# Performance work log

Hardware: AMD Instinct MI355X
Metric: run time of the kernel (lower is better)

The kernel has to match this reference:

```python
import jax, jax.numpy as jnp
import numpy as np

DIM = 384
DIM_HEAD = 32
HEADS = DIM // DIM_HEAD  # 12
WIN = 8
DIM_FF = 1536
FUSED = DIM + DIM + DIM_FF  # 2304


def setup_inputs() -> dict:
    key = jax.random.key(0)
    ks = jax.random.split(key, 8)
    B, H, W = 16, 64, 64
    x = jax.random.normal(ks[0], (B, DIM, H, W), dtype=jnp.float32)
    s = lambda fan_in: 1.0 / np.sqrt(fan_in)
    w_fused = jax.random.normal(ks[1], (FUSED, DIM), dtype=jnp.float32) * s(DIM)
    w_gate = jax.random.normal(ks[2], (HEADS, DIM), dtype=jnp.float32) * s(DIM)
    b_gate = jnp.full((HEADS,), 0.5, dtype=jnp.float32)  # init_constant_(0.5)
    w_attn_out = jax.random.normal(ks[3], (DIM, DIM), dtype=jnp.float32) * s(DIM)
    w_ff_out = jax.random.normal(ks[4], (DIM, DIM_FF), dtype=jnp.float32) * s(DIM_FF)
    # StarReLU learnable scalars (metaformer defaults)
    sr_scale = jnp.asarray(0.8944, dtype=jnp.float32)
    sr_bias = jnp.asarray(-0.4472, dtype=jnp.float32)
    return {"x": x, "w_fused": w_fused, "w_gate": w_gate, "b_gate": b_gate,
            "w_attn_out": w_attn_out, "w_ff_out": w_ff_out,
            "sr_scale": sr_scale, "sr_bias": sr_bias}


def reference(x, w_fused, w_gate, b_gate, w_attn_out, w_ff_out, sr_scale, sr_bias):
    B, C, H, W = x.shape
    p = WIN
    gh, gw = H // p, W // p
    n = p * p
    # b c (h p1) (w p2) -> (b h w) (p1 p2) c
    xw = x.reshape(B, C, gh, p, gw, p).transpose(0, 2, 4, 3, 5, 1).reshape(B * gh * gw, n, C)
    fused = jnp.einsum('bnc,fc->bnf', xw, w_fused)  # [Bw, n, 2304]
    q, kv, x_ff = jnp.split(fused, [DIM, 2 * DIM], axis=-1)
    # b n (h d) -> b h n d
    q = q.reshape(-1, n, HEADS, DIM_HEAD).transpose(0, 2, 1, 3)
    kv = kv.reshape(-1, n, HEADS, DIM_HEAD).transpose(0, 2, 1, 3)
    scale = 1.0 / np.sqrt(DIM_HEAD)
    scores = jnp.einsum('bhnd,bhmd->bhnm', q, kv) * scale
    attn = jax.nn.softmax(scores, axis=-1)
    x_attn = jnp.einsum('bhnm,bhmd->bhnd', attn, kv)  # kv is both key and value
    gate = jnp.einsum('bnc,hc->bnh', xw, w_gate) + b_gate  # [Bw, n, heads]
    x_attn = x_attn * jax.nn.sigmoid(gate.transpose(0, 2, 1)[..., None])
    x_attn = x_attn.transpose(0, 2, 1, 3).reshape(-1, n, DIM)
    ff = sr_scale * jnp.square(jax.nn.relu(x_ff)) + sr_bias  # StarReLU
    out = jnp.einsum('bnc,oc->bno', x_attn, w_attn_out) + jnp.einsum('bnf,of->bno', ff, w_ff_out)
    # (b h w) (p1 p2) c -> b c (h p1) (w p2)
    out = out.reshape(B, gh, gw, p, p, C).transpose(0, 5, 1, 3, 2, 4).reshape(B, C, H, W)
    return out
```

## Files before the change

kernel.cpp:

```cpp
#include <hip/hip_runtime.h>
#include <hip/hip_bf16.h>

typedef __bf16 bf16x8 __attribute__((ext_vector_type(8), may_alias));
typedef float f32x4 __attribute__((ext_vector_type(4), may_alias));
typedef unsigned short ushort_a __attribute__((may_alias));

#define MFMA(a, b, c) __builtin_amdgcn_mfma_f32_16x16x32_bf16(a, b, c, 0, 0, 0)

__device__ __forceinline__ unsigned short f2bf(float f) {
  return __builtin_bit_cast(unsigned short, (__bf16)f);
}


__global__ __launch_bounds__(256) void prep_weights(
    const float* __restrict__ wf, const float* __restrict__ wg,
    const float* __restrict__ wao, const float* __restrict__ wfo,
    unsigned short* __restrict__ ws) {
  int i = blockIdx.x * 256 + threadIdx.x;
  if (i < 884736) { ws[i] = f2bf(wf[i]); return; }
  int j = i - 884736;
  if (j < 6144) { ws[i] = f2bf(j < 4608 ? wg[j] : 0.0f); return; }
  j -= 6144;
  if (j < 147456) { ws[i] = f2bf(wao[j]); return; }
  j -= 147456;
  if (j < 589824) ws[i] = f2bf(wfo[j]);
}


__global__ __launch_bounds__(512, 2) void fused_main(
    const float* __restrict__ x,
    const float* __restrict__ bgate,
    const float* __restrict__ srs,
    const float* __restrict__ srb,
    const unsigned short* __restrict__ wsb,
    float* __restrict__ out) {
  const unsigned short* wfB  = wsb;
  const unsigned short* wgB  = wsb + 884736;
  const unsigned short* waoB = wsb + 890880;
  const unsigned short* wfoB = wsb + 1038336;

  __shared__ __align__(16) char smem[114688];
  char* As  = smem;
  char* Stg = smem + 98304;

  const int tid = threadIdx.x;
  const int lane = tid & 63, wave = tid >> 6;
  const int l15 = lane & 15, l4 = lane >> 4;
  const int pair = wave >> 1, nb = (wave & 1) * 32;
  char* PB  = smem + 49152 + pair * 12288;
  char* KTb = PB + 8192;

  const int g  = blockIdx.x;
  const int wi = (g & 7) * 128 + (g >> 3);
  const int b = wi >> 6, ghi = (wi >> 3) & 7, gwi = wi & 7;
  const int h0 = ghi * 8, w0 = gwi * 8;

  {
    const float* xb = x + (size_t)b * 1572864 + h0 * 64 + w0;
    for (int it = 0; it < 6; ++it) {
      int idx = it * 512 + tid;
      int c = idx % 384, p1 = idx / 384;
      const float* src = xb + (size_t)c * 4096 + p1 * 64;
      float4 v0 = *(const float4*)src;
      float4 v1 = *(const float4*)(src + 4);
      float f[8] = {v0.x, v0.y, v0.z, v0.w, v1.x, v1.y, v1.z, v1.w};
#pragma unroll
      for (int jj = 0; jj < 8; ++jj) {
        int row = p1 * 8 + jj;
        int byte = (row * 768 + c * 2) ^ ((row & 7) << 4);
        *(ushort_a*)(As + byte) = f2bf(f[jj]);
      }
    }
  }
  const float ss = srs[0], sbi = srb[0];
  __syncthreads();

  auto ldA = [&](int row, int ks) -> bf16x8 {
    int byte = (row * 768 + ks * 64 + l4 * 16) ^ ((row & 7) << 4);
    return *(const bf16x8*)(As + byte);
  };

  f32x4 gfr[2] = {};
  {
    const unsigned short* wg0 = wgB + (size_t)l15 * 384 + l4 * 8;
#pragma unroll 2
    for (int ks = 0; ks < 12; ++ks) {
      bf16x8 bg = *(const bf16x8*)(wg0 + ks * 32);
      bf16x8 a0 = ldA(nb + l15, ks), a1 = ldA(nb + 16 + l15, ks);
      gfr[0] = MFMA(a0, bg, gfr[0]);
      gfr[1] = MFMA(a1, bg, gfr[1]);
    }
    float gb = (l15 < 12) ? bgate[l15] : 0.0f;
    gfr[0] += gb;
    gfr[1] += gb;
  }

  f32x4 of[4][3] = {};

#pragma unroll 1
  for (int r = 0; r < 3; ++r) {
    const int h = r * 4 + pair;
    f32x4 qf[2][2] = {}, kf[2][2] = {};
    const unsigned short* wq = wfB + ((size_t)(h * 32) + l15) * 384 + l4 * 8;
    const unsigned short* wk = wq + (size_t)384 * 384;
#pragma unroll 2
    for (int ks = 0; ks < 12; ++ks) {
      bf16x8 a0 = ldA(nb + l15, ks), a1 = ldA(nb + 16 + l15, ks);
#pragma unroll
      for (int nt = 0; nt < 2; ++nt) {
        bf16x8 bq = *(const bf16x8*)(wq + (size_t)nt * 16 * 384 + ks * 32);
        bf16x8 bk = *(const bf16x8*)(wk + (size_t)nt * 16 * 384 + ks * 32);
        qf[0][nt] = MFMA(a0, bq, qf[0][nt]);
        qf[1][nt] = MFMA(a1, bq, qf[1][nt]);
        kf[0][nt] = MFMA(a0, bk, kf[0][nt]);
        kf[1][nt] = MFMA(a1, bk, kf[1][nt]);
      }
    }
#pragma unroll
    for (int mt = 0; mt < 2; ++mt)
#pragma unroll
      for (int nt = 0; nt < 2; ++nt)
#pragma unroll
        for (int rr = 0; rr < 4; ++rr) {
          int n = nb + mt * 16 + l4 * 4 + rr;
          int d = nt * 16 + l15;
          int sw = (n & 7) << 4;
          *(ushort_a*)(PB + ((n * 128 + d * 2) ^ sw)) =
              f2bf(qf[mt][nt][rr] * 0.176776695f);
          unsigned short kvv = f2bf(kf[mt][nt][rr]);
          *(ushort_a*)(PB + ((n * 128 + 64 + d * 2) ^ sw)) = kvv;
          *(ushort_a*)(KTb + ((d * 128 + n * 2) ^ ((d & 7) << 4))) = kvv;
        }
    __syncthreads();
    f32x4 sf[2][4] = {};
    {
      bf16x8 bkv[4];
#pragma unroll
      for (int ni = 0; ni < 4; ++ni) {
        int m = ni * 16 + l15;
        bkv[ni] = *(const bf16x8*)(PB + ((m * 128 + 64 + l4 * 16) ^ ((m & 7) << 4)));
      }
#pragma unroll
      for (int mt = 0; mt < 2; ++mt) {
        int n = nb + mt * 16 + l15;
        bf16x8 aq = *(const bf16x8*)(PB + ((n * 128 + l4 * 16) ^ ((n & 7) << 4)));
#pragma unroll
        for (int ni = 0; ni < 4; ++ni) sf[mt][ni] = MFMA(aq, bkv[ni], sf[mt][ni]);
      }
    }
    __syncthreads();
#pragma unroll
    for (int mt = 0; mt < 2; ++mt) {
#pragma unroll
      for (int rr = 0; rr < 4; ++rr) {
        float v0 = sf[mt][0][rr], v1 = sf[mt][1][rr],
              v2 = sf[mt][2][rr], v3 = sf[mt][3][rr];
        float mx = fmaxf(fmaxf(v0, v1), fmaxf(v2, v3));
        mx = fmaxf(mx, __shfl_xor(mx, 1, 64));
        mx = fmaxf(mx, __shfl_xor(mx, 2, 64));
        mx = fmaxf(mx, __shfl_xor(mx, 4, 64));
        mx = fmaxf(mx, __shfl_xor(mx, 8, 64));
        float e0 = __expf(v0 - mx), e1 = __expf(v1 - mx),
              e2 = __expf(v2 - mx), e3 = __expf(v3 - mx);
        float sm = e0 + e1 + e2 + e3;
        sm += __shfl_xor(sm, 1, 64);
        sm += __shfl_xor(sm, 2, 64);
        sm += __shfl_xor(sm, 4, 64);
        sm += __shfl_xor(sm, 8, 64);
        float rs = 1.0f / sm;
        int n = nb + mt * 16 + l4 * 4 + rr;
        int base = n * 128, sw = (n & 7) << 4;
        *(ushort_a*)(PB + ((base + l15 * 2) ^ sw))      = f2bf(e0 * rs);
        *(ushort_a*)(PB + ((base + 32 + l15 * 2) ^ sw)) = f2bf(e1 * rs);
        *(ushort_a*)(PB + ((base + 64 + l15 * 2) ^ sw)) = f2bf(e2 * rs);
        *(ushort_a*)(PB + ((base + 96 + l15 * 2) ^ sw)) = f2bf(e3 * rs);
      }
    }
    f32x4 xo[2][2] = {};
#pragma unroll
    for (int ks = 0; ks < 2; ++ks) {
      bf16x8 bv[2];
#pragma unroll
      for (int nt = 0; nt < 2; ++nt) {
        int d = nt * 16 + l15;
        bv[nt] = *(const bf16x8*)(KTb + ((d * 128 + ks * 64 + l4 * 16) ^ ((d & 7) << 4)));
      }
#pragma unroll
      for (int mt = 0; mt < 2; ++mt) {
        int n = nb + mt * 16 + l15;
        bf16x8 ap = *(const bf16x8*)(PB + ((n * 128 + ks * 64 + l4 * 16) ^ ((n & 7) << 4)));
        xo[mt][0] = MFMA(ap, bv[0], xo[mt][0]);
        xo[mt][1] = MFMA(ap, bv[1], xo[mt][1]);
      }
    }
#pragma unroll
    for (int mt = 0; mt < 2; ++mt) {
#pragma unroll
      for (int rr = 0; rr < 4; ++rr) {
        float gv = __shfl(gfr[mt][rr], (lane & 48) | h, 64);
        float sg = 1.0f / (1.0f + __expf(-gv));
        int n = nb + mt * 16 + l4 * 4 + rr;
        int sw = (n & 7) << 4;
        int c0 = pair * 32 + l15;
        *(ushort_a*)(Stg + ((n * 256 + c0 * 2) ^ sw))        = f2bf(xo[mt][0][rr] * sg);
        *(ushort_a*)(Stg + ((n * 256 + (c0 + 16) * 2) ^ sw)) = f2bf(xo[mt][1][rr] * sg);
      }
    }
    __syncthreads();
    {
      const unsigned short* wao0 =
          waoB + (size_t)(wave * 48 + l15) * 384 + r * 128 + l4 * 8;
#pragma unroll
      for (int ks = 0; ks < 4; ++ks) {
        int kb = ks * 64 + l4 * 16, sz = (l15 & 7) << 4;
        bf16x8 a0 = *(const bf16x8*)(Stg + ((l15 * 256 + kb) ^ sz));
        bf16x8 a1 = *(const bf16x8*)(Stg + (((16 + l15) * 256 + kb) ^ sz));
        bf16x8 a2 = *(const bf16x8*)(Stg + (((32 + l15) * 256 + kb) ^ sz));
        bf16x8 a3 = *(const bf16x8*)(Stg + (((48 + l15) * 256 + kb) ^ sz));
#pragma unroll
        for (int nt = 0; nt < 3; ++nt) {
          bf16x8 bw = *(const bf16x8*)(wao0 + (size_t)nt * 16 * 384 + ks * 32);
          of[0][nt] = MFMA(a0, bw, of[0][nt]);
          of[1][nt] = MFMA(a1, bw, of[1][nt]);
          of[2][nt] = MFMA(a2, bw, of[2][nt]);
          of[3][nt] = MFMA(a3, bw, of[3][nt]);
        }
      }
    }
  }

#pragma unroll 1
  for (int t = 0; t < 12; ++t) {
    f32x4 ffr[4] = {};
    const unsigned short* wfin =
        wfB + (size_t)(768 + t * 128 + wave * 16 + l15) * 384 + l4 * 8;
#pragma unroll 2
    for (int ks = 0; ks < 12; ++ks) {
      bf16x8 a0 = ldA(l15, ks), a1 = ldA(16 + l15, ks),
             a2 = ldA(32 + l15, ks), a3 = ldA(48 + l15, ks);
      bf16x8 bw = *(const bf16x8*)(wfin + ks * 32);
      ffr[0] = MFMA(a0, bw, ffr[0]);
      ffr[1] = MFMA(a1, bw, ffr[1]);
      ffr[2] = MFMA(a2, bw, ffr[2]);
      ffr[3] = MFMA(a3, bw, ffr[3]);
    }
    char* fb = smem + 49152 + (t & 1) * 16384;
#pragma unroll
    for (int mt = 0; mt < 4; ++mt)
#pragma unroll
      for (int rr = 0; rr < 4; ++rr) {
        float v = fmaxf(ffr[mt][rr], 0.0f);
        v = ss * v * v + sbi;
        int n = mt * 16 + l4 * 4 + rr;
        int cw = wave * 16 + l15;
        *(ushort_a*)(fb + ((n * 256 + cw * 2) ^ ((n & 7) << 4))) = f2bf(v);
      }
    __syncthreads();
    const unsigned short* wfo2 =
        wfoB + (size_t)(wave * 48 + l15) * 1536 + t * 128 + l4 * 8;
#pragma unroll
    for (int ks = 0; ks < 4; ++ks) {
      int kb = ks * 64 + l4 * 16, sz = (l15 & 7) << 4;
      bf16x8 a0 = *(const bf16x8*)(fb + ((l15 * 256 + kb) ^ sz));
      bf16x8 a1 = *(const bf16x8*)(fb + (((16 + l15) * 256 + kb) ^ sz));
      bf16x8 a2 = *(const bf16x8*)(fb + (((32 + l15) * 256 + kb) ^ sz));
      bf16x8 a3 = *(const bf16x8*)(fb + (((48 + l15) * 256 + kb) ^ sz));
#pragma unroll
      for (int nt = 0; nt < 3; ++nt) {
        bf16x8 bw = *(const bf16x8*)(wfo2 + (size_t)nt * 16 * 1536 + ks * 32);
        of[0][nt] = MFMA(a0, bw, of[0][nt]);
        of[1][nt] = MFMA(a1, bw, of[1][nt]);
        of[2][nt] = MFMA(a2, bw, of[2][nt]);
        of[3][nt] = MFMA(a3, bw, of[3][nt]);
      }
    }
  }

  float* ob = out + (size_t)b * 1572864 + h0 * 64 + w0;
#pragma unroll
  for (int nt = 0; nt < 3; ++nt) {
    int col = wave * 48 + nt * 16 + l15;
    float* oc = ob + (size_t)col * 4096;
#pragma unroll
    for (int mt = 0; mt < 4; ++mt) {
      int n0 = mt * 16 + l4 * 4;
      *(f32x4*)(oc + (n0 >> 3) * 64 + (n0 & 7)) = of[mt][nt];
    }
  }
}

extern "C" void kernel_launch(void* const* d_in, const int* in_sizes, int n_in,
                              void* d_out, int out_size, void* d_ws, size_t ws_size,
                              hipStream_t stream) {
  const float* x   = (const float*)d_in[0];
  const float* wf  = (const float*)d_in[1];
  const float* wg  = (const float*)d_in[2];
  const float* bg  = (const float*)d_in[3];
  const float* wao = (const float*)d_in[4];
  const float* wfo = (const float*)d_in[5];
  const float* srs = (const float*)d_in[6];
  const float* srb = (const float*)d_in[7];
  unsigned short* ws = (unsigned short*)d_ws;

  prep_weights<<<6360, 256, 0, stream>>>(wf, wg, wao, wfo, ws);
  fused_main<<<1024, 512, 0, stream>>>(x, bg, srs, srb, ws, (float*)d_out);
}
```

Measured before the change: 563.8 us.

## Repartition waves to two heads per round and shrink LDS for higher occupancy

Attention now assigns four waves per head, each handling 16 rows, and processes two heads per round over six rounds instead of four heads over three. The staging buffer shrinks to 64 columns per round, cutting shared memory from 112KB to 80KB, and launch bounds are raised to allow more blocks per CU. The output projection tiles change to 32 rows by 96 columns per wave, which cuts LDS A-fragment reads but doubles the weight fragments loaded per wave. This costs more rounds and barriers for the attention part and may add register pressure under the tighter launch bound.

```diff
diff --git a/kernel.cpp b/kernel.cpp
--- a/kernel.cpp
+++ b/kernel.cpp
@@ -27,7 +27,7 @@
 }
 
 
-__global__ __launch_bounds__(512, 2) void fused_main(
+__global__ __launch_bounds__(512, 4) void fused_main(
     const float* __restrict__ x,
     const float* __restrict__ bgate,
     const float* __restrict__ srs,
@@ -39,15 +39,17 @@
   const unsigned short* waoB = wsb + 890880;
   const unsigned short* wfoB = wsb + 1038336;
 
-  __shared__ __align__(16) char smem[114688];
+  __shared__ __align__(16) char smem[81920];
   char* As  = smem;
-  char* Stg = smem + 98304;
+  char* Stg = smem + 73728;
 
   const int tid = threadIdx.x;
   const int lane = tid & 63, wave = tid >> 6;
   const int l15 = lane & 15, l4 = lane >> 4;
-  const int pair = wave >> 1, nb = (wave & 1) * 32;
-  char* PB  = smem + 49152 + pair * 12288;
+  const int quad = wave >> 2;
+  const int nb = (wave & 3) * 16;
+  const int rh = wave & 1, cg = wave >> 1;
+  char* PB  = smem + 49152 + quad * 12288;
   char* KTb = PB + 8192;
 
   const int g  = blockIdx.x;
@@ -80,59 +82,53 @@
     return *(const bf16x8*)(As + byte);
   };
 
-  f32x4 gfr[2] = {};
+  f32x4 gfr = {};
   {
     const unsigned short* wg0 = wgB + (size_t)l15 * 384 + l4 * 8;
 #pragma unroll 2
     for (int ks = 0; ks < 12; ++ks) {
       bf16x8 bg = *(const bf16x8*)(wg0 + ks * 32);
-      bf16x8 a0 = ldA(nb + l15, ks), a1 = ldA(nb + 16 + l15, ks);
-      gfr[0] = MFMA(a0, bg, gfr[0]);
-      gfr[1] = MFMA(a1, bg, gfr[1]);
+      bf16x8 a0 = ldA(nb + l15, ks);
+      gfr = MFMA(a0, bg, gfr);
     }
     float gb = (l15 < 12) ? bgate[l15] : 0.0f;
-    gfr[0] += gb;
-    gfr[1] += gb;
-  }
-
-  f32x4 of[4][3] = {};
+    gfr += gb;
+  }
+
+  f32x4 of[2][6] = {};
 
 #pragma unroll 1
-  for (int r = 0; r < 3; ++r) {
-    const int h = r * 4 + pair;
-    f32x4 qf[2][2] = {}, kf[2][2] = {};
+  for (int r = 0; r < 6; ++r) {
+    const int h = r * 2 + quad;
+    f32x4 qf[2] = {}, kf[2] = {};
     const unsigned short* wq = wfB + ((size_t)(h * 32) + l15) * 384 + l4 * 8;
     const unsigned short* wk = wq + (size_t)384 * 384;
 #pragma unroll 2
     for (int ks = 0; ks < 12; ++ks) {
-      bf16x8 a0 = ldA(nb + l15, ks), a1 = ldA(nb + 16 + l15, ks);
+      bf16x8 a0 = ldA(nb + l15, ks);
 #pragma unroll
       for (int nt = 0; nt < 2; ++nt) {
         bf16x8 bq = *(const bf16x8*)(wq + (size_t)nt * 16 * 384 + ks * 32);
         bf16x8 bk = *(const bf16x8*)(wk + (size_t)nt * 16 * 384 + ks * 32);
-        qf[0][nt] = MFMA(a0, bq, qf[0][nt]);
-        qf[1][nt] = MFMA(a1, bq, qf[1][nt]);
-        kf[0][nt] = MFMA(a0, bk, kf[0][nt]);
-        kf[1][nt] = MFMA(a1, bk, kf[1][nt]);
-      }
-    }
-#pragma unroll
-    for (int mt = 0; mt < 2; ++mt)
-#pragma unroll
-      for (int nt = 0; nt < 2; ++nt)
-#pragma unroll
-        for (int rr = 0; rr < 4; ++rr) {
-          int n = nb + mt * 16 + l4 * 4 + rr;
-          int d = nt * 16 + l15;
-          int sw = (n & 7) << 4;
-          *(ushort_a*)(PB + ((n * 128 + d * 2) ^ sw)) =
-              f2bf(qf[mt][nt][rr] * 0.176776695f);
-          unsigned short kvv = f2bf(kf[mt][nt][rr]);
-          *(ushort_a*)(PB + ((n * 128 + 64 + d * 2) ^ sw)) = kvv;
-          *(ushort_a*)(KTb + ((d * 128 + n * 2) ^ ((d & 7) << 4))) = kvv;
-        }
-    __syncthreads();
-    f32x4 sf[2][4] = {};
+        qf[nt] = MFMA(a0, bq, qf[nt]);
+        kf[nt] = MFMA(a0, bk, kf[nt]);
+      }
+    }
+#pragma unroll
+    for (int nt = 0; nt < 2; ++nt)
+#pragma unroll
+      for (int rr = 0; rr < 4; ++rr) {
+        int n = nb + l4 * 4 + rr;
+        int d = nt * 16 + l15;
+        int sw = (n & 7) << 4;
+        *(ushort_a*)(PB + ((n * 128 + d * 2) ^ sw)) =
+            f2bf(qf[nt][rr] * 0.176776695f);
+        unsigned short kvv = f2bf(kf[nt][rr]);
+        *(ushort_a*)(PB + ((n * 128 + 64 + d * 2) ^ sw)) = kvv;
+        *(ushort_a*)(KTb + ((d * 128 + n * 2) ^ ((d & 7) << 4))) = kvv;
+      }
+    __syncthreads();
+    f32x4 sf[4];
     {
       bf16x8 bkv[4];
 #pragma unroll
@@ -140,43 +136,36 @@
         int m = ni * 16 + l15;
         bkv[ni] = *(const bf16x8*)(PB + ((m * 128 + 64 + l4 * 16) ^ ((m & 7) << 4)));
       }
-#pragma unroll
-      for (int mt = 0; mt < 2; ++mt) {
-        int n = nb + mt * 16 + l15;
-        bf16x8 aq = *(const bf16x8*)(PB + ((n * 128 + l4 * 16) ^ ((n & 7) << 4)));
-#pragma unroll
-        for (int ni = 0; ni < 4; ++ni) sf[mt][ni] = MFMA(aq, bkv[ni], sf[mt][ni]);
-      }
-    }
-    __syncthreads();
-#pragma unroll
-    for (int mt = 0; mt < 2; ++mt) {
-#pragma unroll
-      for (int rr = 0; rr < 4; ++rr) {
-        float v0 = sf[mt][0][rr], v1 = sf[mt][1][rr],
-              v2 = sf[mt][2][rr], v3 = sf[mt][3][rr];
-        float mx = fmaxf(fmaxf(v0, v1), fmaxf(v2, v3));
-        mx = fmaxf(mx, __shfl_xor(mx, 1, 64));
-        mx = fmaxf(mx, __shfl_xor(mx, 2, 64));
-        mx = fmaxf(mx, __shfl_xor(mx, 4, 64));
-        mx = fmaxf(mx, __shfl_xor(mx, 8, 64));
-        float e0 = __expf(v0 - mx), e1 = __expf(v1 - mx),
-              e2 = __expf(v2 - mx), e3 = __expf(v3 - mx);
-        float sm = e0 + e1 + e2 + e3;
-        sm += __shfl_xor(sm, 1, 64);
-        sm += __shfl_xor(sm, 2, 64);
-        sm += __shfl_xor(sm, 4, 64);
-        sm += __shfl_xor(sm, 8, 64);
-        float rs = 1.0f / sm;
-        int n = nb + mt * 16 + l4 * 4 + rr;
-        int base = n * 128, sw = (n & 7) << 4;
-        *(ushort_a*)(PB + ((base + l15 * 2) ^ sw))      = f2bf(e0 * rs);
-        *(ushort_a*)(PB + ((base + 32 + l15 * 2) ^ sw)) = f2bf(e1 * rs);
-        *(ushort_a*)(PB + ((base + 64 + l15 * 2) ^ sw)) = f2bf(e2 * rs);
-        *(ushort_a*)(PB + ((base + 96 + l15 * 2) ^ sw)) = f2bf(e3 * rs);
-      }
-    }
-    f32x4 xo[2][2] = {};
+      int n = nb + l15;
+      bf16x8 aq = *(const bf16x8*)(PB + ((n * 128 + l4 * 16) ^ ((n & 7) << 4)));
+#pragma unroll
+      for (int ni = 0; ni < 4; ++ni) sf[ni] = MFMA(aq, bkv[ni], {});
+    }
+    __syncthreads();
+#pragma unroll
+    for (int rr = 0; rr < 4; ++rr) {
+      float v0 = sf[0][rr], v1 = sf[1][rr], v2 = sf[2][rr], v3 = sf[3][rr];
+      float mx = fmaxf(fmaxf(v0, v1), fmaxf(v2, v3));
+      mx = fmaxf(mx, __shfl_xor(mx, 1, 64));
+      mx = fmaxf(mx, __shfl_xor(mx, 2, 64));
+      mx = fmaxf(mx, __shfl_xor(mx, 4, 64));
+      mx = fmaxf(mx, __shfl_xor(mx, 8, 64));
+      float e0 = __expf(v0 - mx), e1 = __expf(v1 - mx),
+            e2 = __expf(v2 - mx), e3 = __expf(v3 - mx);
+      float sm = e0 + e1 + e2 + e3;
+      sm += __shfl_xor(sm, 1, 64);
+      sm += __shfl_xor(sm, 2, 64);
+      sm += __shfl_xor(sm, 4, 64);
+      sm += __shfl_xor(sm, 8, 64);
+      float rs = 1.0f / sm;
+      int n = nb + l4 * 4 + rr;
+      int base = n * 128, sw = (n & 7) << 4;
+      *(ushort_a*)(PB + ((base + l15 * 2) ^ sw))      = f2bf(e0 * rs);
+      *(ushort_a*)(PB + ((base + 32 + l15 * 2) ^ sw)) = f2bf(e1 * rs);
+      *(ushort_a*)(PB + ((base + 64 + l15 * 2) ^ sw)) = f2bf(e2 * rs);
+      *(ushort_a*)(PB + ((base + 96 + l15 * 2) ^ sw)) = f2bf(e3 * rs);
+    }
+    f32x4 xo[2] = {};
 #pragma unroll
     for (int ks = 0; ks < 2; ++ks) {
       bf16x8 bv[2];
@@ -185,45 +174,36 @@
         int d = nt * 16 + l15;
         bv[nt] = *(const bf16x8*)(KTb + ((d * 128 + ks * 64 + l4 * 16) ^ ((d & 7) << 4)));
       }
-#pragma unroll
-      for (int mt = 0; mt < 2; ++mt) {
-        int n = nb + mt * 16 + l15;
-        bf16x8 ap = *(const bf16x8*)(PB + ((n * 128 + ks * 64 + l4 * 16) ^ ((n & 7) << 4)));
-        xo[mt][0] = MFMA(ap, bv[0], xo[mt][0]);
-        xo[mt][1] = MFMA(ap, bv[1], xo[mt][1]);
-      }
-    }
-#pragma unroll
-    for (int mt = 0; mt < 2; ++mt) {
-#pragma unroll
-      for (int rr = 0; rr < 4; ++rr) {
-        float gv = __shfl(gfr[mt][rr], (lane & 48) | h, 64);
-        float sg = 1.0f / (1.0f + __expf(-gv));
-        int n = nb + mt * 16 + l4 * 4 + rr;
-        int sw = (n & 7) << 4;
-        int c0 = pair * 32 + l15;
-        *(ushort_a*)(Stg + ((n * 256 + c0 * 2) ^ sw))        = f2bf(xo[mt][0][rr] * sg);
-        *(ushort_a*)(Stg + ((n * 256 + (c0 + 16) * 2) ^ sw)) = f2bf(xo[mt][1][rr] * sg);
-      }
+      int n = nb + l15;
+      bf16x8 ap = *(const bf16x8*)(PB + ((n * 128 + ks * 64 + l4 * 16) ^ ((n & 7) << 4)));
+      xo[0] = MFMA(ap, bv[0], xo[0]);
+      xo[1] = MFMA(ap, bv[1], xo[1]);
+    }
+#pragma unroll
+    for (int rr = 0; rr < 4; ++rr) {
+      float gv = __shfl(gfr[rr], (lane & 48) | h, 64);
+      float sg = 1.0f / (1.0f + __expf(-gv));
+      int n = nb + l4 * 4 + rr;
+      int sw = (n & 7) << 4;
+      int c0 = quad * 32 + l15;
+      *(ushort_a*)(Stg + ((n * 128 + c0 * 2) ^ sw))        = f2bf(xo[0][rr] * sg);
+      *(ushort_a*)(Stg + ((n * 128 + (c0 + 16) * 2) ^ sw)) = f2bf(xo[1][rr] * sg);
     }
     __syncthreads();
     {
       const unsigned short* wao0 =
-          waoB + (size_t)(wave * 48 + l15) * 384 + r * 128 + l4 * 8;
-#pragma unroll
-      for (int ks = 0; ks < 4; ++ks) {
-        int kb = ks * 64 + l4 * 16, sz = (l15 & 7) << 4;
-        bf16x8 a0 = *(const bf16x8*)(Stg + ((l15 * 256 + kb) ^ sz));
-        bf16x8 a1 = *(const bf16x8*)(Stg + (((16 + l15) * 256 + kb) ^ sz));
-        bf16x8 a2 = *(const bf16x8*)(Stg + (((32 + l15) * 256 + kb) ^ sz));
-        bf16x8 a3 = *(const bf16x8*)(Stg + (((48 + l15) * 256 + kb) ^ sz));
-#pragma unroll
-        for (int nt = 0; nt < 3; ++nt) {
+          waoB + (size_t)(cg * 96 + l15) * 384 + r * 64 + l4 * 8;
+#pragma unroll
+      for (int ks = 0; ks < 2; ++ks) {
+        int kb = ks * 64 + l4 * 16;
+        int r0 = rh * 32 + l15, r1 = rh * 32 + 16 + l15;
+        bf16x8 a0 = *(const bf16x8*)(Stg + ((r0 * 128 + kb) ^ ((r0 & 7) << 4)));
+        bf16x8 a1 = *(const bf16x8*)(Stg + ((r1 * 128 + kb) ^ ((r1 & 7) << 4)));
+#pragma unroll
+        for (int nt = 0; nt < 6; ++nt) {
           bf16x8 bw = *(const bf16x8*)(wao0 + (size_t)nt * 16 * 384 + ks * 32);
           of[0][nt] = MFMA(a0, bw, of[0][nt]);
           of[1][nt] = MFMA(a1, bw, of[1][nt]);
-          of[2][nt] = MFMA(a2, bw, of[2][nt]);
-          of[3][nt] = MFMA(a3, bw, of[3][nt]);
         }
       }
     }
@@ -257,33 +237,30 @@
       }
     __syncthreads();
     const unsigned short* wfo2 =
-        wfoB + (size_t)(wave * 48 + l15) * 1536 + t * 128 + l4 * 8;
+        wfoB + (size_t)(cg * 96 + l15) * 1536 + t * 128 + l4 * 8;
 #pragma unroll
     for (int ks = 0; ks < 4; ++ks) {
-      int kb = ks * 64 + l4 * 16, sz = (l15 & 7) << 4;
-      bf16x8 a0 = *(const bf16x8*)(fb + ((l15 * 256 + kb) ^ sz));
-      bf16x8 a1 = *(const bf16x8*)(fb + (((16 + l15) * 256 + kb) ^ sz));
-      bf16x8 a2 = *(const bf16x8*)(fb + (((32 + l15) * 256 + kb) ^ sz));
-      bf16x8 a3 = *(const bf16x8*)(fb + (((48 + l15) * 256 + kb) ^ sz));
-#pragma unroll
-      for (int nt = 0; nt < 3; ++nt) {
+      int kb = ks * 64 + l4 * 16;
+      int r0 = rh * 32 + l15, r1 = rh * 32 + 16 + l15;
+      bf16x8 a0 = *(const bf16x8*)(fb + ((r0 * 256 + kb) ^ ((r0 & 7) << 4)));
+      bf16x8 a1 = *(const bf16x8*)(fb + ((r1 * 256 + kb) ^ ((r1 & 7) << 4)));
+#pragma unroll
+      for (int nt = 0; nt < 6; ++nt) {
         bf16x8 bw = *(const bf16x8*)(wfo2 + (size_t)nt * 16 * 1536 + ks * 32);
         of[0][nt] = MFMA(a0, bw, of[0][nt]);
         of[1][nt] = MFMA(a1, bw, of[1][nt]);
-        of[2][nt] = MFMA(a2, bw, of[2][nt]);
-        of[3][nt] = MFMA(a3, bw, of[3][nt]);
       }
     }
   }
 
   float* ob = out + (size_t)b * 1572864 + h0 * 64 + w0;
 #pragma unroll
-  for (int nt = 0; nt < 3; ++nt) {
-    int col = wave * 48 + nt * 16 + l15;
+  for (int nt = 0; nt < 6; ++nt) {
+    int col = cg * 96 + nt * 16 + l15;
     float* oc = ob + (size_t)col * 4096;
 #pragma unroll
-    for (int mt = 0; mt < 4; ++mt) {
-      int n0 = mt * 16 + l4 * 4;
+    for (int mt = 0; mt < 2; ++mt) {
+      int n0 = rh * 32 + mt * 16 + l4 * 4;
       *(f32x4*)(oc + (n0 >> 3) * 64 + (n0 & 7)) = of[mt][nt];
     }
   }
```

Result: slower. 831.3 us (+47.4%).

## Process two attention windows per block to halve weight reloads

Applied to the files above, without the earlier changes.

Each block now handles two adjacent 8x8 windows (128 tokens) instead of one, so every weight fragment loaded from global/L2 feeds twice as many MFMAs in the QKV, gate, out-projection and FF GEMMs. The grid shrinks to 512 blocks, LDS grows to 144 KB and the output accumulators double to 8x3 tiles per wave. This cuts weight traffic per token but raises register pressure and LDS use, likely dropping occupancy to one block per CU, and adds extra barriers because buffers are no longer double-buffered.

```diff
diff --git a/kernel.cpp b/kernel.cpp
--- a/kernel.cpp
+++ b/kernel.cpp
@@ -39,34 +39,38 @@
   const unsigned short* waoB = wsb + 890880;
   const unsigned short* wfoB = wsb + 1038336;
 
-  __shared__ __align__(16) char smem[114688];
+  __shared__ __align__(16) char smem[147456];
   char* As  = smem;
   char* Stg = smem + 98304;
+  char* fb  = smem + 98304;
 
   const int tid = threadIdx.x;
   const int lane = tid & 63, wave = tid >> 6;
   const int l15 = lane & 15, l4 = lane >> 4;
-  const int pair = wave >> 1, nb = (wave & 1) * 32;
-  char* PB  = smem + 49152 + pair * 12288;
+  const int p = wave >> 1;
+  const int s = wave & 1;
+  char* PB  = smem + 98304 + p * 12288;
   char* KTb = PB + 8192;
 
   const int g  = blockIdx.x;
-  const int wi = (g & 7) * 128 + (g >> 3);
-  const int b = wi >> 6, ghi = (wi >> 3) & 7, gwi = wi & 7;
-  const int h0 = ghi * 8, w0 = gwi * 8;
+  const int wp = (g & 7) * 64 + (g >> 3);
+  const int b = wp >> 5, rem = wp & 31;
+  const int ghi = rem >> 2, gwq = rem & 3;
+  const int h0 = ghi * 8, w0 = gwq * 16;
 
   {
     const float* xb = x + (size_t)b * 1572864 + h0 * 64 + w0;
-    for (int it = 0; it < 6; ++it) {
+    for (int it = 0; it < 12; ++it) {
       int idx = it * 512 + tid;
-      int c = idx % 384, p1 = idx / 384;
-      const float* src = xb + (size_t)c * 4096 + p1 * 64;
+      int c = idx % 384, pg = idx / 384;
+      int w2 = pg >> 3, p1 = pg & 7;
+      const float* src = xb + (size_t)c * 4096 + p1 * 64 + w2 * 8;
       float4 v0 = *(const float4*)src;
       float4 v1 = *(const float4*)(src + 4);
       float f[8] = {v0.x, v0.y, v0.z, v0.w, v1.x, v1.y, v1.z, v1.w};
 #pragma unroll
       for (int jj = 0; jj < 8; ++jj) {
-        int row = p1 * 8 + jj;
+        int row = w2 * 64 + p1 * 8 + jj;
         int byte = (row * 768 + c * 2) ^ ((row & 7) << 4);
         *(ushort_a*)(As + byte) = f2bf(f[jj]);
       }
@@ -80,26 +84,31 @@
     return *(const bf16x8*)(As + byte);
   };
 
-  f32x4 gfr[2] = {};
+  f32x4 gfr[4] = {};
   {
     const unsigned short* wg0 = wgB + (size_t)l15 * 384 + l4 * 8;
 #pragma unroll 2
     for (int ks = 0; ks < 12; ++ks) {
       bf16x8 bg = *(const bf16x8*)(wg0 + ks * 32);
-      bf16x8 a0 = ldA(nb + l15, ks), a1 = ldA(nb + 16 + l15, ks);
-      gfr[0] = MFMA(a0, bg, gfr[0]);
-      gfr[1] = MFMA(a1, bg, gfr[1]);
+#pragma unroll
+      for (int j4 = 0; j4 < 4; ++j4) {
+        int row = (j4 >> 1) * 64 + s * 32 + (j4 & 1) * 16 + l15;
+        bf16x8 a = ldA(row, ks);
+        gfr[j4] = MFMA(a, bg, gfr[j4]);
+      }
     }
     float gb = (l15 < 12) ? bgate[l15] : 0.0f;
-    gfr[0] += gb;
-    gfr[1] += gb;
-  }
-
-  f32x4 of[4][3] = {};
+#pragma unroll
+    for (int j4 = 0; j4 < 4; ++j4) gfr[j4] += gb;
+  }
+
+  f32x4 of[8][3] = {};
 
 #pragma unroll 1
-  for (int r = 0; r < 3; ++r) {
-    const int h = r * 4 + pair;
+  for (int r = 0; r < 6; ++r) {
+    const int W = r / 3, hr = r - W * 3;
+    const int h = hr * 4 + p;
+    const int nb = W * 64 + s * 32;
     f32x4 qf[2][2] = {}, kf[2][2] = {};
     const unsigned short* wq = wfB + ((size_t)(h * 32) + l15) * 384 + l4 * 8;
     const unsigned short* wk = wq + (size_t)384 * 384;
@@ -122,17 +131,17 @@
       for (int nt = 0; nt < 2; ++nt)
 #pragma unroll
         for (int rr = 0; rr < 4; ++rr) {
-          int n = nb + mt * 16 + l4 * 4 + rr;
+          int nl = s * 32 + mt * 16 + l4 * 4 + rr;
           int d = nt * 16 + l15;
-          int sw = (n & 7) << 4;
-          *(ushort_a*)(PB + ((n * 128 + d * 2) ^ sw)) =
+          int sw = (nl & 7) << 4;
+          *(ushort_a*)(PB + ((nl * 128 + d * 2) ^ sw)) =
               f2bf(qf[mt][nt][rr] * 0.176776695f);
           unsigned short kvv = f2bf(kf[mt][nt][rr]);
-          *(ushort_a*)(PB + ((n * 128 + 64 + d * 2) ^ sw)) = kvv;
-          *(ushort_a*)(KTb + ((d * 128 + n * 2) ^ ((d & 7) << 4))) = kvv;
+          *(ushort_a*)(PB + ((nl * 128 + 64 + d * 2) ^ sw)) = kvv;
+          *(ushort_a*)(KTb + ((d * 128 + nl * 2) ^ ((d & 7) << 4))) = kvv;
         }
     __syncthreads();
-    f32x4 sf[2][4] = {};
+    f32x4 sf[2][4];
     {
       bf16x8 bkv[4];
 #pragma unroll
@@ -142,10 +151,10 @@
       }
 #pragma unroll
       for (int mt = 0; mt < 2; ++mt) {
-        int n = nb + mt * 16 + l15;
+        int n = s * 32 + mt * 16 + l15;
         bf16x8 aq = *(const bf16x8*)(PB + ((n * 128 + l4 * 16) ^ ((n & 7) << 4)));
 #pragma unroll
-        for (int ni = 0; ni < 4; ++ni) sf[mt][ni] = MFMA(aq, bkv[ni], sf[mt][ni]);
+        for (int ni = 0; ni < 4; ++ni) sf[mt][ni] = MFMA(aq, bkv[ni], {});
       }
     }
     __syncthreads();
@@ -168,8 +177,8 @@
         sm += __shfl_xor(sm, 4, 64);
         sm += __shfl_xor(sm, 8, 64);
         float rs = 1.0f / sm;
-        int n = nb + mt * 16 + l4 * 4 + rr;
-        int base = n * 128, sw = (n & 7) << 4;
+        int nl = s * 32 + mt * 16 + l4 * 4 + rr;
+        int base = nl * 128, sw = (nl & 7) << 4;
         *(ushort_a*)(PB + ((base + l15 * 2) ^ sw))      = f2bf(e0 * rs);
         *(ushort_a*)(PB + ((base + 32 + l15 * 2) ^ sw)) = f2bf(e1 * rs);
         *(ushort_a*)(PB + ((base + 64 + l15 * 2) ^ sw)) = f2bf(e2 * rs);
@@ -187,29 +196,30 @@
       }
 #pragma unroll
       for (int mt = 0; mt < 2; ++mt) {
-        int n = nb + mt * 16 + l15;
+        int n = s * 32 + mt * 16 + l15;
         bf16x8 ap = *(const bf16x8*)(PB + ((n * 128 + ks * 64 + l4 * 16) ^ ((n & 7) << 4)));
         xo[mt][0] = MFMA(ap, bv[0], xo[mt][0]);
         xo[mt][1] = MFMA(ap, bv[1], xo[mt][1]);
       }
     }
+    __syncthreads();
 #pragma unroll
     for (int mt = 0; mt < 2; ++mt) {
 #pragma unroll
       for (int rr = 0; rr < 4; ++rr) {
-        float gv = __shfl(gfr[mt][rr], (lane & 48) | h, 64);
+        float gv = __shfl(gfr[W * 2 + mt][rr], (lane & 48) | h, 64);
         float sg = 1.0f / (1.0f + __expf(-gv));
-        int n = nb + mt * 16 + l4 * 4 + rr;
-        int sw = (n & 7) << 4;
-        int c0 = pair * 32 + l15;
-        *(ushort_a*)(Stg + ((n * 256 + c0 * 2) ^ sw))        = f2bf(xo[mt][0][rr] * sg);
-        *(ushort_a*)(Stg + ((n * 256 + (c0 + 16) * 2) ^ sw)) = f2bf(xo[mt][1][rr] * sg);
+        int nl = s * 32 + mt * 16 + l4 * 4 + rr;
+        int sw = (nl & 7) << 4;
+        int c0 = p * 32 + l15;
+        *(ushort_a*)(Stg + ((nl * 256 + c0 * 2) ^ sw))        = f2bf(xo[mt][0][rr] * sg);
+        *(ushort_a*)(Stg + ((nl * 256 + (c0 + 16) * 2) ^ sw)) = f2bf(xo[mt][1][rr] * sg);
       }
     }
     __syncthreads();
     {
       const unsigned short* wao0 =
-          waoB + (size_t)(wave * 48 + l15) * 384 + r * 128 + l4 * 8;
+          waoB + (size_t)(wave * 48 + l15) * 384 + hr * 128 + l4 * 8;
 #pragma unroll
       for (int ks = 0; ks < 4; ++ks) {
         int kb = ks * 64 + l4 * 16, sz = (l15 & 7) << 4;
@@ -220,33 +230,32 @@
 #pragma unroll
         for (int nt = 0; nt < 3; ++nt) {
           bf16x8 bw = *(const bf16x8*)(wao0 + (size_t)nt * 16 * 384 + ks * 32);
-          of[0][nt] = MFMA(a0, bw, of[0][nt]);
-          of[1][nt] = MFMA(a1, bw, of[1][nt]);
-          of[2][nt] = MFMA(a2, bw, of[2][nt]);
-          of[3][nt] = MFMA(a3, bw, of[3][nt]);
+          of[W * 4 + 0][nt] = MFMA(a0, bw, of[W * 4 + 0][nt]);
+          of[W * 4 + 1][nt] = MFMA(a1, bw, of[W * 4 + 1][nt]);
+          of[W * 4 + 2][nt] = MFMA(a2, bw, of[W * 4 + 2][nt]);
+          of[W * 4 + 3][nt] = MFMA(a3, bw, of[W * 4 + 3][nt]);
         }
       }
     }
+    __syncthreads();
   }
 
 #pragma unroll 1
   for (int t = 0; t < 12; ++t) {
-    f32x4 ffr[4] = {};
+    f32x4 ffr[8] = {};
     const unsigned short* wfin =
         wfB + (size_t)(768 + t * 128 + wave * 16 + l15) * 384 + l4 * 8;
 #pragma unroll 2
     for (int ks = 0; ks < 12; ++ks) {
-      bf16x8 a0 = ldA(l15, ks), a1 = ldA(16 + l15, ks),
-             a2 = ldA(32 + l15, ks), a3 = ldA(48 + l15, ks);
       bf16x8 bw = *(const bf16x8*)(wfin + ks * 32);
-      ffr[0] = MFMA(a0, bw, ffr[0]);
-      ffr[1] = MFMA(a1, bw, ffr[1]);
-      ffr[2] = MFMA(a2, bw, ffr[2]);
-      ffr[3] = MFMA(a3, bw, ffr[3]);
-    }
-    char* fb = smem + 49152 + (t & 1) * 16384;
-#pragma unroll
-    for (int mt = 0; mt < 4; ++mt)
+#pragma unroll
+      for (int mt = 0; mt < 8; ++mt) {
+        bf16x8 a = ldA(mt * 16 + l15, ks);
+        ffr[mt] = MFMA(a, bw, ffr[mt]);
+      }
+    }
+#pragma unroll
+    for (int mt = 0; mt < 8; ++mt)
 #pragma unroll
       for (int rr = 0; rr < 4; ++rr) {
         float v = fmaxf(ffr[mt][rr], 0.0f);
@@ -261,19 +270,17 @@
 #pragma unroll
     for (int ks = 0; ks < 4; ++ks) {
       int kb = ks * 64 + l4 * 16, sz = (l15 & 7) << 4;
-      bf16x8 a0 = *(const bf16x8*)(fb + ((l15 * 256 + kb) ^ sz));
-      bf16x8 a1 = *(const bf16x8*)(fb + (((16 + l15) * 256 + kb) ^ sz));
-      bf16x8 a2 = *(const bf16x8*)(fb + (((32 + l15) * 256 + kb) ^ sz));
-      bf16x8 a3 = *(const bf16x8*)(fb + (((48 + l15) * 256 + kb) ^ sz));
 #pragma unroll
       for (int nt = 0; nt < 3; ++nt) {
         bf16x8 bw = *(const bf16x8*)(wfo2 + (size_t)nt * 16 * 1536 + ks * 32);
-        of[0][nt] = MFMA(a0, bw, of[0][nt]);
-        of[1][nt] = MFMA(a1, bw, of[1][nt]);
-        of[2][nt] = MFMA(a2, bw, of[2][nt]);
-        of[3][nt] = MFMA(a3, bw, of[3][nt]);
-      }
-    }
+#pragma unroll
+        for (int mt = 0; mt < 8; ++mt) {
+          bf16x8 a = *(const bf16x8*)(fb + (((mt * 16 + l15) * 256 + kb) ^ sz));
+          of[mt][nt] = MFMA(a, bw, of[mt][nt]);
+        }
+      }
+    }
+    __syncthreads();
   }
 
   float* ob = out + (size_t)b * 1572864 + h0 * 64 + w0;
@@ -282,9 +289,10 @@
     int col = wave * 48 + nt * 16 + l15;
     float* oc = ob + (size_t)col * 4096;
 #pragma unroll
-    for (int mt = 0; mt < 4; ++mt) {
-      int n0 = mt * 16 + l4 * 4;
-      *(f32x4*)(oc + (n0 >> 3) * 64 + (n0 & 7)) = of[mt][nt];
+    for (int mt = 0; mt < 8; ++mt) {
+      int w2 = mt >> 2;
+      int n0 = (mt & 3) * 16 + l4 * 4;
+      *(f32x4*)(oc + (n0 >> 3) * 64 + (n0 & 7) + w2 * 8) = of[mt][nt];
     }
   }
 }
@@ -303,5 +311,5 @@
   unsigned short* ws = (unsigned short*)d_ws;
 
   prep_weights<<<6360, 256, 0, stream>>>(wf, wg, wao, wfo, ws);
-  fused_main<<<1024, 512, 0, stream>>>(x, bg, srs, srb, ws, (float*)d_out);
+  fused_main<<<512, 512, 0, stream>>>(x, bg, srs, srb, ws, (float*)d_out);
 }
```

After: 624.2 us. 10.7% more time.
